# Kernel tuning notes

Measured on AMD Instinct MI355X. Metric: run time of the kernel, lower is better.

Reference implementation:

```python
import jax, jax.numpy as jnp
import numpy as np

ALPHA = 0.8
GAMMA = 2.0
SMOOTH = 1e-4
FOCAL_W = 20.0
DICE_W = 1.0
IOU_W = 1.0
MASK_THRESH = 0.0
AREA_RANGES = np.array([[0.0, 0.04], [0.01, 0.16], [0.09, 0.49], [0.25, 1.0]], dtype=np.float32)
B, K, H, W = 128, 4, 256, 256


def setup_inputs() -> dict:
    key = jax.random.key(0)
    k1, k2, k3, k4 = jax.random.split(key, 4)
    pred_masks = jax.random.normal(k1, (B, K, H, W), dtype=jnp.float32)
    pred_ious = jax.random.uniform(k2, (B, K), dtype=jnp.float32)
    # binary targets with varying per-sample foreground density so different
    # samples fall into different area_ranges (exercises the branching)
    dens = jax.random.uniform(k3, (B, 1, 1, 1), dtype=jnp.float32)
    noise = jax.random.uniform(k4, (B, 1, H, W), dtype=jnp.float32)
    targets = (noise < dens).astype(jnp.float32)
    return {"pred_masks": pred_masks, "pred_ious": pred_ious, "targets": targets}


def _aggregate(loss_bk, valid_bk):
    # per-sample mean over valid idxs, then mean over samples with >=1 valid idx
    cnt = valid_bk.sum(axis=1)                                   # [B]
    per_sample = (loss_bk * valid_bk).sum(axis=1) / jnp.maximum(cnt, 1.0)
    per_sample = jnp.where(cnt > 0, per_sample, 0.0)
    vb = (cnt > 0).astype(loss_bk.dtype).sum()
    total = per_sample.sum()
    return jnp.where(vb > 0, total / jnp.maximum(vb, 1.0), total)


def _compute(pred_masks, pred_ious, targets):
    b = pred_masks.shape[0]
    x = pred_masks.reshape(b, K, -1)                             # [B,K,HW] logits
    t = targets.reshape(b, -1)                                   # [B,HW] binary
    hw = t.shape[1]
    ratio = t.sum(axis=1) / float(hw)                            # [B]
    lo = jnp.asarray(AREA_RANGES[:, 0])
    hi = jnp.asarray(AREA_RANGES[:, 1])
    valid = ((ratio[:, None] > lo[None, :]) & (ratio[:, None] < hi[None, :])).astype(x.dtype)  # [B,K]

    tb = t[:, None, :]                                           # [B,1,HW]
    # focal: stable BCE-with-logits, elementwise
    bce = jnp.maximum(x, 0.0) - x * tb + jnp.log1p(jnp.exp(-jnp.abs(x)))
    focal_bk = (ALPHA * (1.0 - jnp.exp(-bce)) ** GAMMA * bce).mean(axis=2)  # [B,K]
    focal = FOCAL_W * _aggregate(focal_bk, valid)

    # dice on clamped sigmoid probabilities
    p = jnp.clip(jax.nn.sigmoid(x), 1e-4, 1.0 - 1e-4)
    inter = (p * tb).sum(axis=2)                                 # [B,K]
    dice_bk = 1.0 - (2.0 * inter + SMOOTH) / (p.sum(axis=2) + t.sum(axis=1)[:, None] + SMOOTH)
    dice = DICE_W * _aggregate(dice_bk, valid)

    # iou prediction loss on thresholded masks
    m = (x >= MASK_THRESH).astype(x.dtype)
    i2 = (m * tb).sum(axis=2)
    iou_gt = (i2 + SMOOTH) / (m.sum(axis=2) + t.sum(axis=1)[:, None] - i2 + SMOOTH)
    iou_bk = (pred_ious - iou_gt) ** 2                           # [B,K]
    iou = IOU_W * _aggregate(iou_bk, valid)

    return focal, dice, iou


def reference(pred_masks, pred_ious, targets):
    focal, dice, iou = _compute(pred_masks, pred_ious, targets)
    return focal, dice, iou
```

## Files before the change

### kernel.cpp

```cpp
#include <hip/hip_runtime.h>
#include <math.h>

#define B_   128
#define K_   4
#define HW_  65536

constexpr int BLOCK = 256;
constexpr int NC    = 16;
constexpr int CHUNK = HW_ / NC;
constexpr int G     = CHUNK / 4 / BLOCK;

typedef float vfloat4 __attribute__((ext_vector_type(4)));

__device__ __forceinline__ void proc_elem(float x, float t,
                                          float& fs, float& in, float& ps,
                                          float& i2, float& ms) {
    float e   = __expf(-fabsf(x));
    float inv = __builtin_amdgcn_rcpf(1.0f + e);
    bool  pos = (x >= 0.0f);
    float s   = pos ? inv : 1.0f - inv;
    float nms = fmaf(-2.0f, s, 1.0f);
    float pt  = fmaf(t, nms, s);
    float l   = __logf(pt);
    float om  = 1.0f - pt;
    fs = fmaf(om * om * l, -0.8f, fs);
    float pc  = fminf(fmaxf(s, 1e-4f), 0.9999f);
    ps += pc;
    in  = fmaf(pc, t, in);
    float m = pos ? 1.0f : 0.0f;
    ms += m;
    i2  = fmaf(m, t, i2);
}

__device__ __forceinline__ void proc4(const vfloat4& xv, const vfloat4& tv,
                                      float& fs, float& in, float& ps,
                                      float& i2, float& ms) {
    proc_elem(xv.x, tv.x, fs, in, ps, i2, ms);
    proc_elem(xv.y, tv.y, fs, in, ps, i2, ms);
    proc_elem(xv.z, tv.z, fs, in, ps, i2, ms);
    proc_elem(xv.w, tv.w, fs, in, ps, i2, ms);
}

__global__ __launch_bounds__(BLOCK, 4) void partial_kernel(
    const float* __restrict__ pred_masks,
    const float* __restrict__ targets,
    float* __restrict__ fsum,
    float* __restrict__ inter,
    float* __restrict__ psum,
    float* __restrict__ i2s,
    float* __restrict__ msum,
    float* __restrict__ tsum)
{
    const int blk = blockIdx.x;
    const int c   = blk & (NC - 1);
    const int b   = blk >> 4;

    const vfloat4* __restrict__ t4 =
        reinterpret_cast<const vfloat4*>(targets + (size_t)b * HW_ + c * CHUNK);
    const float*  xb = pred_masks + (size_t)b * K_ * HW_ + c * CHUNK;
    const vfloat4* __restrict__ x0 = reinterpret_cast<const vfloat4*>(xb);
    const vfloat4* __restrict__ x1 = reinterpret_cast<const vfloat4*>(xb + HW_);
    const vfloat4* __restrict__ x2 = reinterpret_cast<const vfloat4*>(xb + 2 * HW_);
    const vfloat4* __restrict__ x3 = reinterpret_cast<const vfloat4*>(xb + 3 * HW_);

    float fs[K_] = {0.f, 0.f, 0.f, 0.f};
    float in[K_] = {0.f, 0.f, 0.f, 0.f};
    float ps[K_] = {0.f, 0.f, 0.f, 0.f};
    float i2[K_] = {0.f, 0.f, 0.f, 0.f};
    float ms[K_] = {0.f, 0.f, 0.f, 0.f};
    float ts = 0.f;

    int idx = threadIdx.x;
    vfloat4 tv  = __builtin_nontemporal_load(&t4[idx]);
    vfloat4 xv0 = __builtin_nontemporal_load(&x0[idx]);
    vfloat4 xv1 = __builtin_nontemporal_load(&x1[idx]);
    vfloat4 xv2 = __builtin_nontemporal_load(&x2[idx]);
    vfloat4 xv3 = __builtin_nontemporal_load(&x3[idx]);

    #pragma unroll
    for (int g = 0; g < G; ++g) {
        vfloat4 ntv, nx0, nx1, nx2, nx3;
        if (g < G - 1) {
            const int nidx = idx + BLOCK;
            ntv = __builtin_nontemporal_load(&t4[nidx]);
            nx0 = __builtin_nontemporal_load(&x0[nidx]);
            nx1 = __builtin_nontemporal_load(&x1[nidx]);
            nx2 = __builtin_nontemporal_load(&x2[nidx]);
            nx3 = __builtin_nontemporal_load(&x3[nidx]);
        }
        proc4(xv0, tv, fs[0], in[0], ps[0], i2[0], ms[0]);
        proc4(xv1, tv, fs[1], in[1], ps[1], i2[1], ms[1]);
        proc4(xv2, tv, fs[2], in[2], ps[2], i2[2], ms[2]);
        proc4(xv3, tv, fs[3], in[3], ps[3], i2[3], ms[3]);
        ts += tv.x + tv.y + tv.z + tv.w;
        if (g < G - 1) {
            idx += BLOCK;
            tv = ntv; xv0 = nx0; xv1 = nx1; xv2 = nx2; xv3 = nx3;
        }
    }

    float vals[21];
    #pragma unroll
    for (int k = 0; k < K_; ++k) {
        vals[k]      = fs[k];
        vals[4 + k]  = in[k];
        vals[8 + k]  = ps[k];
        vals[12 + k] = i2[k];
        vals[16 + k] = ms[k];
    }
    vals[20] = ts;

    const int lane = threadIdx.x & 63;
    const int wave = threadIdx.x >> 6;

    #pragma unroll
    for (int v = 0; v < 21; ++v) {
        float x = vals[v];
        #pragma unroll
        for (int off = 32; off > 0; off >>= 1) x += __shfl_down(x, off, 64);
        vals[v] = x;
    }

    __shared__ float smem[21 * 4];
    if (lane == 0) {
        #pragma unroll
        for (int v = 0; v < 21; ++v) smem[v * 4 + wave] = vals[v];
    }
    __syncthreads();

    if (threadIdx.x < 21) {
        const int v = threadIdx.x;
        const float x = smem[v * 4 + 0] + smem[v * 4 + 1] +
                        smem[v * 4 + 2] + smem[v * 4 + 3];
        float* dst;
        if      (v < 4)  dst = &fsum[b * K_ + v];
        else if (v < 8)  dst = &inter[b * K_ + (v - 4)];
        else if (v < 12) dst = &psum[b * K_ + (v - 8)];
        else if (v < 16) dst = &i2s[b * K_ + (v - 12)];
        else if (v < 20) dst = &msum[b * K_ + (v - 16)];
        else             dst = &tsum[b];
        atomicAdd(dst, x);
    }
}

__global__ __launch_bounds__(128) void finalize_kernel(
    const float* __restrict__ pred_ious,
    const float* __restrict__ fsum,
    const float* __restrict__ inter,
    const float* __restrict__ psum,
    const float* __restrict__ i2s,
    const float* __restrict__ msum,
    const float* __restrict__ tsum,
    float* __restrict__ out)
{
    const float lo[K_] = {0.00f, 0.01f, 0.09f, 0.25f};
    const float hi[K_] = {0.04f, 0.16f, 0.49f, 1.00f};
    const float SMOOTH = 0.0001f;

    const int b = threadIdx.x;
    const float ts = tsum[b];
    const float ratio = ts * (1.0f / (float)HW_);

    float cnt = 0.f, fA = 0.f, dA = 0.f, iA = 0.f;
    #pragma unroll
    for (int k = 0; k < K_; ++k) {
        const bool valid = (ratio > lo[k]) && (ratio < hi[k]);
        if (valid) {
            cnt += 1.0f;
            fA += fsum[b * K_ + k] * (1.0f / (float)HW_);
            const float in_ = inter[b * K_ + k];
            const float ps_ = psum[b * K_ + k];
            dA += 1.0f - (2.0f * in_ + SMOOTH) / (ps_ + ts + SMOOTH);
            const float i2_ = i2s[b * K_ + k];
            const float ms_ = msum[b * K_ + k];
            const float gt  = (i2_ + SMOOTH) / (ms_ + ts - i2_ + SMOOTH);
            const float d   = pred_ious[b * K_ + k] - gt;
            iA += d * d;
        }
    }
    const float invc = (cnt > 0.f) ? (1.0f / cnt) : 0.0f;
    fA *= invc; dA *= invc; iA *= invc;
    float vb = (cnt > 0.f) ? 1.0f : 0.0f;

    float vals[4] = {fA, dA, iA, vb};
    const int lane = threadIdx.x & 63;
    const int wave = threadIdx.x >> 6;
    #pragma unroll
    for (int v = 0; v < 4; ++v) {
        float x = vals[v];
        #pragma unroll
        for (int off = 32; off > 0; off >>= 1) x += __shfl_down(x, off, 64);
        vals[v] = x;
    }
    __shared__ float smem[4 * 2];
    if (lane == 0) {
        #pragma unroll
        for (int v = 0; v < 4; ++v) smem[v * 2 + wave] = vals[v];
    }
    __syncthreads();
    if (threadIdx.x == 0) {
        const float fT  = smem[0] + smem[1];
        const float dT  = smem[2] + smem[3];
        const float iT  = smem[4] + smem[5];
        const float vbT = smem[6] + smem[7];
        const float scale = (vbT > 0.f) ? (1.0f / vbT) : 1.0f;
        out[0] = 20.0f * fT * scale;
        out[1] = dT * scale;
        out[2] = iT * scale;
    }
}

extern "C" void kernel_launch(void* const* d_in, const int* in_sizes, int n_in,
                              void* d_out, int out_size, void* d_ws, size_t ws_size,
                              hipStream_t stream) {
    const float* pred_masks = (const float*)d_in[0];
    const float* pred_ious  = (const float*)d_in[1];
    const float* targets    = (const float*)d_in[2];
    float* out = (float*)d_out;

    float* ws    = (float*)d_ws;
    float* fsum  = ws;
    float* inter = ws + 512;
    float* psum  = ws + 1024;
    float* i2s   = ws + 1536;
    float* msum  = ws + 2048;
    float* tsum  = ws + 2560;

    (void)hipMemsetAsync(d_ws, 0, 2688 * sizeof(float), stream);

    partial_kernel<<<B_ * NC, BLOCK, 0, stream>>>(
        pred_masks, targets, fsum, inter, psum, i2s, msum, tsum);
    finalize_kernel<<<1, 128, 0, stream>>>(
        pred_ious, fsum, inter, psum, i2s, msum, tsum, out);
}
```

Baseline: 214.8 us.

## Stage inputs through double-buffered LDS using global_load_lds DMA

Replaces the per-thread register double-buffered nontemporal vector loads with 16-byte global_load_lds transfers into a two-stage LDS buffer, one stage per 1024 elements. Each stage is read back from LDS after a block barrier while the next stage is in flight. The aim is to free VGPRs and let the loads stream asynchronously. In exchange it adds one block barrier per stage, extra LDS reads, and about 40 KB of LDS per block. Correctness depends on the barrier also waiting for the outstanding DMA loads.

```diff
diff --git a/kernel.cpp b/kernel.cpp
--- a/kernel.cpp
+++ b/kernel.cpp
@@ -1,16 +1,25 @@
 #include <hip/hip_runtime.h>
 #include <math.h>
+#include <stdint.h>
 
 #define B_   128
 #define K_   4
 #define HW_  65536
 
-constexpr int BLOCK = 256;
-constexpr int NC    = 16;
-constexpr int CHUNK = HW_ / NC;
-constexpr int G     = CHUNK / 4 / BLOCK;
+constexpr int BLOCK  = 256;
+constexpr int NC     = 16;
+constexpr int CHUNK  = HW_ / NC;
+constexpr int STAGE  = BLOCK * 4;
+constexpr int NSTAGE = CHUNK / STAGE;
 
 typedef float vfloat4 __attribute__((ext_vector_type(4)));
+
+__device__ __forceinline__ void dma16(const float* g, float* l) {
+    __builtin_amdgcn_global_load_lds(
+        (__attribute__((address_space(1))) void*)(uintptr_t)(void*)(const_cast<float*>(g)),
+        (__attribute__((address_space(3))) void*)(uint32_t)(uintptr_t)(void*)l,
+        16, 0, 0);
+}
 
 __device__ __forceinline__ void proc_elem(float x, float t,
                                           float& fs, float& in, float& ps,
@@ -51,17 +60,29 @@
     float* __restrict__ msum,
     float* __restrict__ tsum)
 {
+    __shared__ float lds[2][5][STAGE];
+
     const int blk = blockIdx.x;
     const int c   = blk & (NC - 1);
     const int b   = blk >> 4;
 
-    const vfloat4* __restrict__ t4 =
-        reinterpret_cast<const vfloat4*>(targets + (size_t)b * HW_ + c * CHUNK);
-    const float*  xb = pred_masks + (size_t)b * K_ * HW_ + c * CHUNK;
-    const vfloat4* __restrict__ x0 = reinterpret_cast<const vfloat4*>(xb);
-    const vfloat4* __restrict__ x1 = reinterpret_cast<const vfloat4*>(xb + HW_);
-    const vfloat4* __restrict__ x2 = reinterpret_cast<const vfloat4*>(xb + 2 * HW_);
-    const vfloat4* __restrict__ x3 = reinterpret_cast<const vfloat4*>(xb + 3 * HW_);
+    const float* tb = targets    + (size_t)b * HW_ + c * CHUNK;
+    const float* xb = pred_masks + (size_t)b * K_ * HW_ + c * CHUNK;
+
+    const int tid  = threadIdx.x;
+    const int wave = tid >> 6;
+    const int lane = tid & 63;
+    const int off0 = tid * 4;
+    float* ldst0 = &lds[0][0][0];
+    (void)ldst0;
+
+    {
+        dma16(tb + off0,            &lds[0][0][wave * 256]);
+        dma16(xb + off0,            &lds[0][1][wave * 256]);
+        dma16(xb + HW_ + off0,      &lds[0][2][wave * 256]);
+        dma16(xb + 2 * HW_ + off0,  &lds[0][3][wave * 256]);
+        dma16(xb + 3 * HW_ + off0,  &lds[0][4][wave * 256]);
+    }
 
     float fs[K_] = {0.f, 0.f, 0.f, 0.f};
     float in[K_] = {0.f, 0.f, 0.f, 0.f};
@@ -70,32 +91,25 @@
     float ms[K_] = {0.f, 0.f, 0.f, 0.f};
     float ts = 0.f;
 
-    int idx = threadIdx.x;
-    vfloat4 tv  = __builtin_nontemporal_load(&t4[idx]);
-    vfloat4 xv0 = __builtin_nontemporal_load(&x0[idx]);
-    vfloat4 xv1 = __builtin_nontemporal_load(&x1[idx]);
-    vfloat4 xv2 = __builtin_nontemporal_load(&x2[idx]);
-    vfloat4 xv3 = __builtin_nontemporal_load(&x3[idx]);
-
-    #pragma unroll
-    for (int g = 0; g < G; ++g) {
-        vfloat4 ntv, nx0, nx1, nx2, nx3;
-        if (g < G - 1) {
-            const int nidx = idx + BLOCK;
-            ntv = __builtin_nontemporal_load(&t4[nidx]);
-            nx0 = __builtin_nontemporal_load(&x0[nidx]);
-            nx1 = __builtin_nontemporal_load(&x1[nidx]);
-            nx2 = __builtin_nontemporal_load(&x2[nidx]);
-            nx3 = __builtin_nontemporal_load(&x3[nidx]);
+    #pragma unroll
+    for (int s = 0; s < NSTAGE; ++s) {
+        __syncthreads();
+        const int buf  = s & 1;
+        const int nbuf = buf ^ 1;
+        if (s + 1 < NSTAGE) {
+            const int gof = (s + 1) * STAGE + off0;
+            dma16(tb + gof,            &lds[nbuf][0][wave * 256]);
+            dma16(xb + gof,            &lds[nbuf][1][wave * 256]);
+            dma16(xb + HW_ + gof,      &lds[nbuf][2][wave * 256]);
+            dma16(xb + 2 * HW_ + gof,  &lds[nbuf][3][wave * 256]);
+            dma16(xb + 3 * HW_ + gof,  &lds[nbuf][4][wave * 256]);
         }
-        proc4(xv0, tv, fs[0], in[0], ps[0], i2[0], ms[0]);
-        proc4(xv1, tv, fs[1], in[1], ps[1], i2[1], ms[1]);
-        proc4(xv2, tv, fs[2], in[2], ps[2], i2[2], ms[2]);
-        proc4(xv3, tv, fs[3], in[3], ps[3], i2[3], ms[3]);
+        const vfloat4 tv = *(const vfloat4*)&lds[buf][0][off0];
         ts += tv.x + tv.y + tv.z + tv.w;
-        if (g < G - 1) {
-            idx += BLOCK;
-            tv = ntv; xv0 = nx0; xv1 = nx1; xv2 = nx2; xv3 = nx3;
+        #pragma unroll
+        for (int k = 0; k < K_; ++k) {
+            const vfloat4 xv = *(const vfloat4*)&lds[buf][1 + k][off0];
+            proc4(xv, tv, fs[k], in[k], ps[k], i2[k], ms[k]);
         }
     }
 
@@ -110,9 +124,6 @@
     }
     vals[20] = ts;
 
-    const int lane = threadIdx.x & 63;
-    const int wave = threadIdx.x >> 6;
-
     #pragma unroll
     for (int v = 0; v < 21; ++v) {
         float x = vals[v];
@@ -122,14 +133,15 @@
     }
 
     __shared__ float smem[21 * 4];
+    __syncthreads();
     if (lane == 0) {
         #pragma unroll
         for (int v = 0; v < 21; ++v) smem[v * 4 + wave] = vals[v];
     }
     __syncthreads();
 
-    if (threadIdx.x < 21) {
-        const int v = threadIdx.x;
+    if (tid < 21) {
+        const int v = tid;
         const float x = smem[v * 4 + 0] + smem[v * 4 + 1] +
                         smem[v * 4 + 2] + smem[v * 4 + 3];
         float* dst;
```

After: 222.5 us. 1.04x slower.
